# Performance work log

Hardware: AMD Instinct MI355X
Metric: run time of the kernel (lower is better)

## Reference

```python
import jax, jax.numpy as jnp
import numpy as np

N = 4096          # nodes (= Mamba sequence length)
E_EDGES = 65536   # edges
D = 512           # dim_h (= d_inner, expand=1)
NEXP = 4          # num_experts (cfg.model.num_experts)
DSTATE = 16
DCONV = 4
DTRANK = 32       # ceil(D/16)
EPS = 1e-5


def _silu(x):
    return x * jax.nn.sigmoid(x)


def _bn(h, g, b):
    # BatchNorm1d over node axis (batch statistics)
    mu = h.mean(0)
    var = h.var(0)
    return (h - mu) * jax.lax.rsqrt(var + EPS) * g + b


def _mamba(u, in_w, conv_w, conv_b, x_w, dt_w, dt_b, A_log, Dp, out_w):
    # u: [L, D] single-sequence Mamba(d_model=D, d_state=16, d_conv=4, expand=1)
    L = u.shape[0]
    xz = u @ in_w                      # [L, 2D]
    xc, z = xz[:, :D], xz[:, D:]
    xp = jnp.pad(xc, ((DCONV - 1, 0), (0, 0)))
    xconv = conv_b
    for k in range(DCONV):             # depthwise causal conv, tiny fixed loop
        xconv = xconv + conv_w[:, k] * xp[k:k + L]
    xs = _silu(xconv)                  # [L, D]
    dbc = xs @ x_w                     # [L, DTRANK + 2*DSTATE]
    dt = jax.nn.softplus(dbc[:, :DTRANK] @ dt_w + dt_b)          # [L, D]
    Bm = dbc[:, DTRANK:DTRANK + DSTATE]                          # [L, S]
    Cm = dbc[:, DTRANK + DSTATE:]                                # [L, S]
    A = -jnp.exp(A_log)                                          # [D, S]
    dA = jnp.exp(dt[:, :, None] * A[None])                       # [L, D, S]
    dBu = dt[:, :, None] * Bm[:, None, :] * xs[:, :, None]       # [L, D, S]

    def step(hprev, inp):
        dA_t, dBu_t, C_t = inp
        hn = dA_t * hprev + dBu_t
        return hn, (hn * C_t[None, :]).sum(-1)

    _, ys = jax.lax.scan(step, jnp.zeros((D, DSTATE), u.dtype), (dA, dBu, Cm))
    y = ys + Dp * xs
    return (y * _silu(z)) @ out_w      # [L, D]


def setup_inputs() -> dict:
    key = jax.random.key(0)
    ks = jax.random.split(key, 24)
    s = 1.0 / np.sqrt(D)
    inp = {}
    inp['x'] = jax.random.normal(ks[0], (N, D), jnp.float32)
    inp['edge_index'] = jax.random.randint(ks[1], (2, E_EDGES), 0, N)
    inp['edge_attr'] = jax.random.normal(ks[2], (E_EDGES, D), jnp.float32)
    # GINE nn: Linear(D,D) -> ReLU -> Linear(D,D)
    inp['gin_w1'] = jax.random.normal(ks[3], (D, D)) * s
    inp['gin_b1'] = jnp.zeros((D,))
    inp['gin_w2'] = jax.random.normal(ks[4], (D, D)) * s
    inp['gin_b2'] = jnp.zeros((D,))
    # BatchNorms
    inp['bn1l_g'] = jnp.ones((D,)); inp['bn1l_b'] = jnp.zeros((D,))
    inp['bn1a_g'] = jnp.ones((D,)); inp['bn1a_b'] = jnp.zeros((D,))
    inp['bn2_g'] = jnp.ones((D,)); inp['bn2_b'] = jnp.zeros((D,))
    # gating MLP [D, D//2, NEXP]
    inp['gate_w1'] = jax.random.normal(ks[5], (D, D // 2)) * s
    inp['gate_b1'] = jnp.zeros((D // 2,))
    inp['gate_w2'] = jax.random.normal(ks[6], (D // 2, NEXP)) * (1.0 / np.sqrt(D // 2))
    inp['gate_b2'] = jnp.zeros((NEXP,))
    # stacked per-expert Mamba params
    inp['in_w'] = jax.random.normal(ks[7], (NEXP, D, 2 * D)) * s
    inp['conv_w'] = jax.random.normal(ks[8], (NEXP, D, DCONV)) * 0.5
    inp['conv_b'] = jnp.zeros((NEXP, D))
    inp['x_w'] = jax.random.normal(ks[9], (NEXP, D, DTRANK + 2 * DSTATE)) * s
    inp['dt_w'] = jax.random.normal(ks[10], (NEXP, DTRANK, D)) * (1.0 / np.sqrt(DTRANK))
    inp['dt_b'] = jax.random.normal(ks[11], (NEXP, D)) * 0.1 - 4.0
    A0 = jnp.log(jnp.arange(1, DSTATE + 1, dtype=jnp.float32))
    inp['A_log'] = jnp.broadcast_to(A0, (NEXP, D, DSTATE)).copy()
    inp['Dp'] = jnp.ones((NEXP, D))
    inp['out_w'] = jax.random.normal(ks[12], (NEXP, D, D)) * s
    # FFN
    inp['ff_w1'] = jax.random.normal(ks[13], (D, 2 * D)) * s
    inp['ff_b1'] = jnp.zeros((2 * D,))
    inp['ff_w2'] = jax.random.normal(ks[14], (2 * D, D)) * (1.0 / np.sqrt(2 * D))
    inp['ff_b2'] = jnp.zeros((D,))
    return inp


def reference(x, edge_index, edge_attr,
              gin_w1, gin_b1, gin_w2, gin_b2,
              bn1l_g, bn1l_b, bn1a_g, bn1a_b, bn2_g, bn2_b,
              gate_w1, gate_b1, gate_w2, gate_b2,
              in_w, conv_w, conv_b, x_w, dt_w, dt_b, A_log, Dp, out_w,
              ff_w1, ff_b1, ff_w2, ff_b2):
    h_in = x
    src, dst = edge_index[0], edge_index[1]
    # local GINEConv: nn(x + sum_j relu(x_j + e_ji))
    msg = jax.nn.relu(x[src] + edge_attr)                      # [E, D]
    aggr = jax.ops.segment_sum(msg, dst, num_segments=N)       # [N, D]
    h_local = jax.nn.relu((x + aggr) @ gin_w1 + gin_b1) @ gin_w2 + gin_b2
    h_local = _bn(h_in + h_local, bn1l_g, bn1l_b)
    # gated mixture of Mamba experts
    gate = jax.nn.softmax(jax.nn.relu(x @ gate_w1 + gate_b1) @ gate_w2 + gate_b2, axis=-1)  # [N, NEXP]
    ys = jax.vmap(_mamba, in_axes=(None, 0, 0, 0, 0, 0, 0, 0, 0, 0))(
        x, in_w, conv_w, conv_b, x_w, dt_w, dt_b, A_log, Dp, out_w)  # [NEXP, N, D]
    h_attn = jnp.einsum('ne,end->nd', gate, ys)
    h_attn = _bn(h_in + h_attn, bn1a_g, bn1a_b)
    # fuse + FFN
    h = h_local + h_attn
    ff = jax.nn.relu(h @ ff_w1 + ff_b1) @ ff_w2 + ff_b2
    return _bn(h + ff, bn2_g, bn2_b)
```

## Files before the change

kernel.cpp:

```cpp
#include <hip/hip_runtime.h>
#include <hip/hip_bf16.h>
#include <math.h>

#define N_NODES 4096
#define E_EDGE 65536
#define D 512
#define NEXP 4
#define DSTATE 16
#define DCONV 4
#define DTRANK 32
#define EPS 1e-5f
#define LCHUNK 64
#define NCHUNK (N_NODES / LCHUNK)

typedef __hip_bfloat16 bf16;
typedef short bf16x8 __attribute__((ext_vector_type(8)));
typedef float f32x4 __attribute__((ext_vector_type(4)));
typedef unsigned short u16x4 __attribute__((ext_vector_type(4)));

__device__ __forceinline__ float siluf(float x) { return x / (1.f + __expf(-x)); }
__device__ __forceinline__ float softplusf(float x) {
  return (x > 20.f) ? x : log1pf(__expf(x));
}
__device__ __forceinline__ unsigned short f2bf(float v) {
  bf16 b = __float2bfloat16(v);
  return *reinterpret_cast<unsigned short*>(&b);
}
__device__ __forceinline__ float bfu2f(unsigned short u) {
  bf16 b;
  *reinterpret_cast<unsigned short*>(&b) = u;
  return __bfloat162float(b);
}

__device__ __forceinline__ void gload16(const void* g, void* l) {
  __builtin_amdgcn_global_load_lds(
      (const __attribute__((address_space(1))) void*)g,
      (__attribute__((address_space(3))) void*)l, 16, 0, 0);
}

template <int FN, int EPI, bool STATS>
__global__ __launch_bounds__(256, 2) void mm_k(
    const bf16* __restrict__ A, int lda, long sA,
    const bf16* __restrict__ Bt, int ldb, long sB,
    const float* __restrict__ bias,
    float* __restrict__ Cf, bf16* __restrict__ Cb, int ldc, long sC, int K,
    const float* __restrict__ part, float* __restrict__ sacc) {
  constexpr int BN = FN * 32;
  __shared__ __align__(16) bf16 As[2][128 * 32];
  __shared__ __align__(16) bf16 Bs[2][BN * 32];
  const int z = blockIdx.z;
  A += (size_t)z * sA;
  Bt += (size_t)z * sB;
  const int tid = threadIdx.x;
  const int w = tid >> 6, l = tid & 63;
  const int wr = w >> 1, wc = w & 1;
  const int bm = blockIdx.y * 128, bn = blockIdx.x * BN;

  f32x4 acc[4][FN];
#pragma unroll
  for (int i = 0; i < 4; ++i)
#pragma unroll
    for (int j = 0; j < FN; ++j) acc[i][j] = 0.f;

  const int srow = l >> 2, schunk = l & 3;
  const bf16* gA = A + (size_t)(bm + w * 16 + srow) * lda + schunk * 8;
  const bf16* gB = Bt + (size_t)(bn + w * 16 + srow) * ldb + schunk * 8;

  const int ar = wr * 64 + (l & 15);
  const int br = wc * FN * 16 + (l & 15);
  const int kb = l >> 4;

  auto stage = [&](int b, int k0) {
    gload16(gA + k0, As[b] + w * 512);
    gload16(gA + k0 + (size_t)64 * lda, As[b] + 64 * 32 + w * 512);
    gload16(gB + k0, Bs[b] + w * 512);
    if (FN == 4) gload16(gB + k0 + (size_t)64 * ldb, Bs[b] + 64 * 32 + w * 512);
  };

  stage(0, 0);
  __syncthreads();
  int cur = 0;
  for (int k0 = 0; k0 < K; k0 += 32) {
    if (k0 + 32 < K) stage(cur ^ 1, k0 + 32);
    const bf16x8* Ap = (const bf16x8*)As[cur];
    const bf16x8* Bp = (const bf16x8*)Bs[cur];
    bf16x8 af[4], bfr[FN];
#pragma unroll
    for (int i = 0; i < 4; ++i) af[i] = Ap[(ar + i * 16) * 4 + kb];
#pragma unroll
    for (int j = 0; j < FN; ++j) bfr[j] = Bp[(br + j * 16) * 4 + kb];
#pragma unroll
    for (int i = 0; i < 4; ++i)
#pragma unroll
      for (int j = 0; j < FN; ++j)
        acc[i][j] = __builtin_amdgcn_mfma_f32_16x16x32_bf16(bfr[j], af[i], acc[i][j], 0, 0, 0);
    __syncthreads();
    cur ^= 1;
  }

  if (Cf) Cf += (size_t)z * sC;
  if (Cb) Cb += (size_t)z * sC;
  const int r0 = bm + wr * 64 + (l & 15);
  const int cb0 = bn + wc * FN * 16 + ((l >> 4) << 2);
  f32x4 ssum[FN], ssq[FN];
  if (STATS) {
#pragma unroll
    for (int j = 0; j < FN; ++j) { ssum[j] = 0.f; ssq[j] = 0.f; }
  }
#pragma unroll
  for (int i = 0; i < 4; ++i) {
    const int row = r0 + i * 16;
#pragma unroll
    for (int j = 0; j < FN; ++j) {
      const int col = cb0 + j * 16;
      f32x4 v = acc[i][j];
      if (bias) v += *(const f32x4*)&bias[col];
      if (EPI == 1) {
#pragma unroll
        for (int r = 0; r < 4; ++r) v[r] = fmaxf(v[r], 0.f);
      }
      if (Cf) *(f32x4*)&Cf[(size_t)row * ldc + col] = v;
      if (Cb) {
        u16x4 u;
#pragma unroll
        for (int r = 0; r < 4; ++r) u[r] = f2bf(v[r]);
        *(u16x4*)&Cb[(size_t)row * ldc + col] = u;
      }
      if (STATS) {
        f32x4 p = *(const f32x4*)&part[(size_t)row * ldc + col];
        f32x4 t = v + p;
        ssum[j] += t;
        ssq[j] += t * t;
      }
    }
  }
  if (STATS) {
#pragma unroll
    for (int m = 1; m < 16; m <<= 1) {
#pragma unroll
      for (int j = 0; j < FN; ++j)
#pragma unroll
        for (int r = 0; r < 4; ++r) {
          ssum[j][r] += __shfl_xor(ssum[j][r], m);
          ssq[j][r] += __shfl_xor(ssq[j][r], m);
        }
    }
    if ((l & 15) == 0) {
#pragma unroll
      for (int j = 0; j < FN; ++j)
#pragma unroll
        for (int r = 0; r < 4; ++r) {
          atomicAdd(&sacc[cb0 + j * 16 + r], ssum[j][r]);
          atomicAdd(&sacc[512 + cb0 + j * 16 + r], ssq[j][r]);
        }
    }
  }
}

__global__ __launch_bounds__(256, 2) void g1pack_k(
    const bf16* __restrict__ hpre, const bf16* __restrict__ xbf,
    const bf16* __restrict__ gw1t, const bf16* __restrict__ catw,
    const float* __restrict__ gin_b1, const float* __restrict__ gate_b1,
    bf16* __restrict__ t1, float* __restrict__ g1, bf16* __restrict__ xz) {
  __shared__ __align__(16) bf16 As[2][128 * 32];
  __shared__ __align__(16) bf16 Bs[2][128 * 32];
  const int b = blockIdx.x;
  const bool isGin = b < 128;
  int bm, bnBase;
  const bf16 *A, *Bt;
  if (isGin) {
    bm = (b >> 2) * 128;
    bnBase = (b & 3) * 128;
    A = hpre;
    Bt = gw1t + (size_t)bnBase * 512;
  } else {
    const int local = b - 128;
    bm = (local / 34) * 128;
    bnBase = (local % 34) * 128;
    A = xbf;
    Bt = catw + (size_t)bnBase * 512;
  }
  const int tid = threadIdx.x;
  const int w = tid >> 6, l = tid & 63;
  const int wr = w >> 1, wc = w & 1;

  f32x4 acc[4][4];
#pragma unroll
  for (int i = 0; i < 4; ++i)
#pragma unroll
    for (int j = 0; j < 4; ++j) acc[i][j] = 0.f;

  const int srow = l >> 2, schunk = l & 3;
  const bf16* gA = A + (size_t)(bm + w * 16 + srow) * 512 + schunk * 8;
  const bf16* gB = Bt + (size_t)(w * 16 + srow) * 512 + schunk * 8;

  const int ar = wr * 64 + (l & 15);
  const int br = wc * 64 + (l & 15);
  const int kb = l >> 4;

  auto stage = [&](int bb, int k0) {
    gload16(gA + k0, As[bb] + w * 512);
    gload16(gA + k0 + (size_t)64 * 512, As[bb] + 64 * 32 + w * 512);
    gload16(gB + k0, Bs[bb] + w * 512);
    gload16(gB + k0 + (size_t)64 * 512, Bs[bb] + 64 * 32 + w * 512);
  };

  stage(0, 0);
  __syncthreads();
  int cur = 0;
  for (int k0 = 0; k0 < 512; k0 += 32) {
    if (k0 + 32 < 512) stage(cur ^ 1, k0 + 32);
    const bf16x8* Ap = (const bf16x8*)As[cur];
    const bf16x8* Bp = (const bf16x8*)Bs[cur];
    bf16x8 af[4], bfr[4];
#pragma unroll
    for (int i = 0; i < 4; ++i) af[i] = Ap[(ar + i * 16) * 4 + kb];
#pragma unroll
    for (int j = 0; j < 4; ++j) bfr[j] = Bp[(br + j * 16) * 4 + kb];
#pragma unroll
    for (int i = 0; i < 4; ++i)
#pragma unroll
      for (int j = 0; j < 4; ++j)
        acc[i][j] = __builtin_amdgcn_mfma_f32_16x16x32_bf16(bfr[j], af[i], acc[i][j], 0, 0, 0);
    __syncthreads();
    cur ^= 1;
  }

  const int r0 = bm + wr * 64 + (l & 15);
  const int c0 = wc * 64 + ((l >> 4) << 2);
  const bool isGate = (!isGin) && (bnBase < 256);
  bf16* xz_e = nullptr;
  int co_base = 0;
  if (!isGin && !isGate) {
    const int e = (bnBase - 256) >> 10;
    xz_e = xz + (size_t)e * N_NODES * 1024;
    co_base = (bnBase - 256) & 1023;
  }
#pragma unroll
  for (int i = 0; i < 4; ++i) {
    const int row = r0 + i * 16;
#pragma unroll
    for (int j = 0; j < 4; ++j) {
      const int ct = c0 + j * 16;
      f32x4 v = acc[i][j];
      if (isGin) {
        const int col = bnBase + ct;
        v += *(const f32x4*)&gin_b1[col];
        u16x4 u;
#pragma unroll
        for (int r = 0; r < 4; ++r) u[r] = f2bf(fmaxf(v[r], 0.f));
        *(u16x4*)&t1[(size_t)row * 512 + col] = u;
      } else if (isGate) {
        const int col = bnBase + ct;
        v += *(const f32x4*)&gate_b1[col];
#pragma unroll
        for (int r = 0; r < 4; ++r) v[r] = fmaxf(v[r], 0.f);
        *(f32x4*)&g1[(size_t)row * 256 + col] = v;
      } else {
        const int co = co_base + ct;
        u16x4 u;
#pragma unroll
        for (int r = 0; r < 4; ++r) u[r] = f2bf(v[r]);
        *(u16x4*)&xz_e[(size_t)row * 1024 + co] = u;
      }
    }
  }
}

struct MmArgs {
  const bf16* A[4];
  const bf16* Bt[4];
  const float* bias[4];
  float* Cf[4];
  bf16* Cb[4];
  const float* part[4];
  float* sacc[4];
  long sA[4], sB[4], sC[4];
  int lda[4], ldb[4], ldc[4], K[4], epi[4], stats[4], gx[4], cum[4];
};
__global__ __launch_bounds__(256, 2) void mgemm_k(MmArgs a) {
  __shared__ __align__(16) bf16 As[2][128 * 32];
  __shared__ __align__(16) bf16 Bs[2][64 * 32];
  int b = blockIdx.x;
  int i = 0;
  while (b >= a.cum[i]) ++i;
  int local = b - (i ? a.cum[i - 1] : 0);
  const int perz = a.gx[i] * 32;
  const int z = local / perz;
  const int rem = local - z * perz;
  const int by = rem / a.gx[i];
  const int bx = rem - by * a.gx[i];
  const int lda = a.lda[i], ldb = a.ldb[i], ldc = a.ldc[i], K = a.K[i];
  const bf16* A = a.A[i] + (size_t)z * a.sA[i];
  const bf16* Bt = a.Bt[i] + (size_t)z * a.sB[i];

  const int tid = threadIdx.x;
  const int w = tid >> 6, l = tid & 63;
  const int wr = w >> 1, wc = w & 1;
  const int bm = by * 128, bn = bx * 64;

  f32x4 acc[4][2];
#pragma unroll
  for (int p = 0; p < 4; ++p)
#pragma unroll
    for (int j = 0; j < 2; ++j) acc[p][j] = 0.f;

  const int srow = l >> 2, schunk = l & 3;
  const bf16* gA = A + (size_t)(bm + w * 16 + srow) * lda + schunk * 8;
  const bf16* gB = Bt + (size_t)(bn + w * 16 + srow) * ldb + schunk * 8;

  const int ar = wr * 64 + (l & 15);
  const int br = wc * 32 + (l & 15);
  const int kb = l >> 4;

  auto stage = [&](int bb, int k0) {
    gload16(gA + k0, As[bb] + w * 512);
    gload16(gA + k0 + (size_t)64 * lda, As[bb] + 64 * 32 + w * 512);
    gload16(gB + k0, Bs[bb] + w * 512);
  };

  stage(0, 0);
  __syncthreads();
  int cur = 0;
  for (int k0 = 0; k0 < K; k0 += 32) {
    if (k0 + 32 < K) stage(cur ^ 1, k0 + 32);
    const bf16x8* Ap = (const bf16x8*)As[cur];
    const bf16x8* Bp = (const bf16x8*)Bs[cur];
    bf16x8 af[4], bfr[2];
#pragma unroll
    for (int p = 0; p < 4; ++p) af[p] = Ap[(ar + p * 16) * 4 + kb];
#pragma unroll
    for (int j = 0; j < 2; ++j) bfr[j] = Bp[(br + j * 16) * 4 + kb];
#pragma unroll
    for (int p = 0; p < 4; ++p)
#pragma unroll
      for (int j = 0; j < 2; ++j)
        acc[p][j] = __builtin_amdgcn_mfma_f32_16x16x32_bf16(bfr[j], af[p], acc[p][j], 0, 0, 0);
    __syncthreads();
    cur ^= 1;
  }

  float* Cf = a.Cf[i] ? a.Cf[i] + (size_t)z * a.sC[i] : nullptr;
  bf16* Cb = a.Cb[i] ? a.Cb[i] + (size_t)z * a.sC[i] : nullptr;
  const float* bias = a.bias[i];
  const int epi = a.epi[i], stats = a.stats[i];
  const int r0 = bm + wr * 64 + (l & 15);
  const int cb0 = bn + wc * 32 + ((l >> 4) << 2);
  f32x4 ssum[2], ssq[2];
  ssum[0] = 0.f; ssum[1] = 0.f; ssq[0] = 0.f; ssq[1] = 0.f;
#pragma unroll
  for (int p = 0; p < 4; ++p) {
    const int row = r0 + p * 16;
#pragma unroll
    for (int j = 0; j < 2; ++j) {
      const int col = cb0 + j * 16;
      f32x4 v = acc[p][j];
      if (bias) v += *(const f32x4*)&bias[col];
      if (epi == 1) {
#pragma unroll
        for (int r = 0; r < 4; ++r) v[r] = fmaxf(v[r], 0.f);
      }
      if (Cf) *(f32x4*)&Cf[(size_t)row * ldc + col] = v;
      if (Cb) {
        u16x4 u;
#pragma unroll
        for (int r = 0; r < 4; ++r) u[r] = f2bf(v[r]);
        *(u16x4*)&Cb[(size_t)row * ldc + col] = u;
      }
      if (stats) {
        f32x4 pp = *(const f32x4*)&a.part[i][(size_t)row * ldc + col];
        f32x4 t = v + pp;
        ssum[j] += t;
        ssq[j] += t * t;
      }
    }
  }
  if (stats) {
#pragma unroll
    for (int m = 1; m < 16; m <<= 1) {
#pragma unroll
      for (int j = 0; j < 2; ++j)
#pragma unroll
        for (int r = 0; r < 4; ++r) {
          ssum[j][r] += __shfl_xor(ssum[j][r], m);
          ssq[j][r] += __shfl_xor(ssq[j][r], m);
        }
    }
    if ((l & 15) == 0) {
#pragma unroll
      for (int j = 0; j < 2; ++j)
#pragma unroll
        for (int r = 0; r < 4; ++r) {
          atomicAdd(&a.sacc[i][cb0 + j * 16 + r], ssum[j][r]);
          atomicAdd(&a.sacc[i][512 + cb0 + j * 16 + r], ssq[j][r]);
        }
    }
  }
}

struct WtArgs {
  const float* in[8];
  bf16* out[8];
  int K[8], N[8], ldo[8];
  long sin[8], sout[8];
  int cum[8];
};
__global__ __launch_bounds__(256) void wtrans_all_k(WtArgs a) {
  __shared__ float t[32][33];
  int b = blockIdx.x;
  int i = 0;
  while (b >= a.cum[i]) ++i;
  int local = b - (i ? a.cum[i - 1] : 0);
  const int ntx = a.N[i] / 32;
  const int nty = a.K[i] / 32;
  const int perz = ntx * nty;
  const int z = local / perz;
  const int rem = local - z * perz;
  const int bx = rem % ntx, by = rem / ntx;
  const float* in = a.in[i] + (size_t)z * a.sin[i];
  bf16* out = a.out[i] + (size_t)z * a.sout[i];
  const int N = a.N[i], ldo = a.ldo[i];
  const int n0 = bx * 32, k0 = by * 32;
  const int tx = threadIdx.x & 31, ty = threadIdx.x >> 5;
  for (int r = ty; r < 32; r += 8) t[r][tx] = in[(size_t)(k0 + r) * N + n0 + tx];
  __syncthreads();
  for (int r = ty; r < 32; r += 8)
    out[(size_t)(n0 + r) * ldo + k0 + tx] = __float2bfloat16(t[tx][r]);
}

__global__ void hist_k(const int* __restrict__ ei, int* __restrict__ deg) {
  int e = blockIdx.x * 256 + threadIdx.x;
  if (e < E_EDGE) atomicAdd(&deg[ei[E_EDGE + e]], 1);
}

__global__ __launch_bounds__(1024) void prefix_k(const int* __restrict__ deg,
                                                 int* __restrict__ rowstart) {
  __shared__ int s[1024];
  int t = threadIdx.x;
  int base = t * 4;
  int d0 = deg[base], d1 = deg[base + 1], d2 = deg[base + 2], d3 = deg[base + 3];
  int sum = d0 + d1 + d2 + d3;
  s[t] = sum;
  __syncthreads();
  for (int off = 1; off < 1024; off <<= 1) {
    int v = (t >= off) ? s[t - off] : 0;
    __syncthreads();
    s[t] += v;
    __syncthreads();
  }
  int excl = s[t] - sum;
  rowstart[base] = excl;
  rowstart[base + 1] = excl + d0;
  rowstart[base + 2] = excl + d0 + d1;
  rowstart[base + 3] = excl + d0 + d1 + d2;
}

__global__ void scatter_k(const int* __restrict__ ei, const int* __restrict__ rowstart,
                          int* __restrict__ cnt, int* __restrict__ eid) {
  int e = blockIdx.x * 256 + threadIdx.x;
  if (e < E_EDGE) {
    int dst = ei[E_EDGE + e];
    int slot = rowstart[dst] + atomicAdd(&cnt[dst], 1);
    eid[slot] = e;
  }
}

__global__ __launch_bounds__(256) void aggr_gather_k(
    const float* __restrict__ x, const int* __restrict__ ei, const float* __restrict__ ea,
    const int* __restrict__ rowstart, const int* __restrict__ deg,
    const int* __restrict__ eid, bf16* __restrict__ hpre, bf16* __restrict__ xbf) {
  __shared__ float comb[512];
  const int n = blockIdx.x;
  const int sub = threadIdx.x >> 7;
  const int lane = threadIdx.x & 127;
  const int d4 = lane << 2;
  const int beg = rowstart[n];
  const int end = beg + deg[n];
  f32x4 a = 0.f;
  for (int i = beg + sub; i < end; i += 2) {
    const int e = eid[i];
    const int s = ei[e];
    f32x4 xv = *(const f32x4*)&x[(size_t)s * D + d4];
    f32x4 ev = *(const f32x4*)&ea[(size_t)e * D + d4];
#pragma unroll
    for (int j = 0; j < 4; ++j) a[j] += fmaxf(xv[j] + ev[j], 0.f);
  }
  if (sub == 0) *(f32x4*)&comb[d4] = a;
  __syncthreads();
  if (sub == 1) {
    a += *(const f32x4*)&comb[d4];
    f32x4 xn = *(const f32x4*)&x[(size_t)n * D + d4];
    u16x4 h, xb;
#pragma unroll
    for (int j = 0; j < 4; ++j) {
      h[j] = f2bf(xn[j] + a[j]);
      xb[j] = f2bf(xn[j]);
    }
    *(u16x4*)&hpre[(size_t)n * D + d4] = h;
    *(u16x4*)&xbf[(size_t)n * D + d4] = xb;
  }
}

__device__ __forceinline__ void gate2_body(const float* __restrict__ g1,
                                           const float* __restrict__ w2,
                                           const float* __restrict__ b2,
                                           float* __restrict__ gate, int blk) {
  int row = blk * 4 + (threadIdx.x >> 6);
  int lane = threadIdx.x & 63;
  float a0 = 0.f, a1 = 0.f, a2 = 0.f, a3 = 0.f;
  for (int k = lane; k < 256; k += 64) {
    float v = g1[(size_t)row * 256 + k];
    a0 = fmaf(v, w2[k * 4 + 0], a0);
    a1 = fmaf(v, w2[k * 4 + 1], a1);
    a2 = fmaf(v, w2[k * 4 + 2], a2);
    a3 = fmaf(v, w2[k * 4 + 3], a3);
  }
#pragma unroll
  for (int off = 32; off; off >>= 1) {
    a0 += __shfl_down(a0, off);
    a1 += __shfl_down(a1, off);
    a2 += __shfl_down(a2, off);
    a3 += __shfl_down(a3, off);
  }
  if (lane == 0) {
    float l0 = a0 + b2[0], l1 = a1 + b2[1], l2 = a2 + b2[2], l3 = a3 + b2[3];
    float m = fmaxf(fmaxf(l0, l1), fmaxf(l2, l3));
    float e0 = __expf(l0 - m), e1 = __expf(l1 - m), e2 = __expf(l2 - m), e3 = __expf(l3 - m);
    float s = 1.f / (e0 + e1 + e2 + e3);
    gate[row * 4 + 0] = e0 * s;
    gate[row * 4 + 1] = e1 * s;
    gate[row * 4 + 2] = e2 * s;
    gate[row * 4 + 3] = e3 * s;
  }
}

__global__ __launch_bounds__(256) void gate2_k(const float* __restrict__ g1,
                                               const float* __restrict__ w2,
                                               const float* __restrict__ b2,
                                               float* __restrict__ gate) {
  gate2_body(g1, w2, b2, gate, blockIdx.x);
}

__device__ __forceinline__ void conv_body(const bf16* __restrict__ xz,
                                          const float* __restrict__ cw,
                                          const float* __restrict__ cb,
                                          bf16* __restrict__ xs, int z, int e0, int bx) {
  xz += (size_t)z * N_NODES * 2 * D;
  xs += (size_t)z * N_NODES * D;
  cw += (size_t)(e0 + z) * D * DCONV;
  cb += (size_t)(e0 + z) * D;
  int idx = bx * 256 + threadIdx.x;
  if (idx >= N_NODES * (D / 4)) return;
  int t = idx >> 7;
  int d4 = (idx & 127) << 2;
  float a[4];
#pragma unroll
  for (int j = 0; j < 4; ++j) a[j] = cb[d4 + j];
#pragma unroll
  for (int k = 0; k < DCONV; ++k) {
    int tt = t + k - (DCONV - 1);
    if (tt >= 0) {
      u16x4 v = *(const u16x4*)&xz[(size_t)tt * (2 * D) + d4];
#pragma unroll
      for (int j = 0; j < 4; ++j) a[j] = fmaf(cw[(d4 + j) * DCONV + k], bfu2f(v[j]), a[j]);
    }
  }
  u16x4 o;
#pragma unroll
  for (int j = 0; j < 4; ++j) o[j] = f2bf(siluf(a[j]));
  *(u16x4*)&xs[(size_t)t * D + d4] = o;
}

__global__ void conv_silu_k(const bf16* __restrict__ xz, const float* __restrict__ cw,
                            const float* __restrict__ cb, bf16* __restrict__ xs, int e0) {
  conv_body(xz, cw, cb, xs, blockIdx.y, e0, blockIdx.x);
}

__global__ __launch_bounds__(256) void convgate_k(
    const bf16* __restrict__ xz, const float* __restrict__ cw,
    const float* __restrict__ cb, bf16* __restrict__ xs,
    const float* __restrict__ g1, const float* __restrict__ w2,
    const float* __restrict__ b2, float* __restrict__ gate) {
  if (blockIdx.y == 4) {
    if (blockIdx.x < N_NODES / 4) gate2_body(g1, w2, b2, gate, blockIdx.x);
    return;
  }
  conv_body(xz, cw, cb, xs, blockIdx.y, 0, blockIdx.x);
}

__device__ __forceinline__ void bn_params(const float* acc, int d, float& mu, float& rsig) {
  mu = acc[d] * (1.f / N_NODES);
  float var = acc[512 + d] * (1.f / N_NODES) - mu * mu;
  rsig = rsqrtf(var + EPS);
}

__global__ void norm_k(const float* __restrict__ p, const bf16* __restrict__ q,
                       const float* __restrict__ acc, const float* __restrict__ g,
                       const float* __restrict__ b, float* __restrict__ o) {
  int idx = blockIdx.x * blockDim.x + threadIdx.x;
  if (idx >= N_NODES * (D / 4)) return;
  int d4 = (idx & 127) << 2;
  size_t base = (size_t)idx << 2;
  f32x4 pv = *(const f32x4*)&p[base];
  u16x4 qv = *(const u16x4*)&q[base];
  f32x4 gv = *(const f32x4*)&g[d4];
  f32x4 bv = *(const f32x4*)&b[d4];
  f32x4 ov;
#pragma unroll
  for (int j = 0; j < 4; ++j) {
    float mu, rs;
    bn_params(acc, d4 + j, mu, rs);
    ov[j] = (pv[j] + bfu2f(qv[j]) - mu) * rs * gv[j] + bv[j];
  }
  *(f32x4*)&o[base] = ov;
}

__global__ void bnadd2_k(const float* __restrict__ x, const bf16* __restrict__ hloc,
                         const bf16* __restrict__ hattn, const float* __restrict__ acc1,
                         const float* __restrict__ acc2, const float* __restrict__ g1,
                         const float* __restrict__ b1, const float* __restrict__ g2,
                         const float* __restrict__ b2, float* __restrict__ of,
                         bf16* __restrict__ ob) {
  int idx = blockIdx.x * blockDim.x + threadIdx.x;
  if (idx >= N_NODES * (D / 4)) return;
  int d4 = (idx & 127) << 2;
  size_t base = (size_t)idx << 2;
  f32x4 xv = *(const f32x4*)&x[base];
  u16x4 hl = *(const u16x4*)&hloc[base];
  u16x4 ha = *(const u16x4*)&hattn[base];
  f32x4 g1v = *(const f32x4*)&g1[d4];
  f32x4 b1v = *(const f32x4*)&b1[d4];
  f32x4 g2v = *(const f32x4*)&g2[d4];
  f32x4 b2v = *(const f32x4*)&b2[d4];
  f32x4 ov;
  u16x4 obv;
#pragma unroll
  for (int j = 0; j < 4; ++j) {
    float mu1, rs1, mu2, rs2;
    bn_params(acc1, d4 + j, mu1, rs1);
    bn_params(acc2, d4 + j, mu2, rs2);
    float v = (xv[j] + bfu2f(hl[j]) - mu1) * rs1 * g1v[j] + b1v[j] +
              (xv[j] + bfu2f(ha[j]) - mu2) * rs2 * g2v[j] + b2v[j];
    ov[j] = v;
    obv[j] = f2bf(v);
  }
  *(f32x4*)&of[base] = ov;
  *(u16x4*)&ob[base] = obv;
}

__global__ __launch_bounds__(512) void scanA_k(const bf16* __restrict__ xs,
                                               const float* __restrict__ dbc,
                                               const float* __restrict__ Alog,
                                               const float* __restrict__ dtw,
                                               const float* __restrict__ dtbias,
                                               bf16* __restrict__ dtout,
                                               bf16* __restrict__ Q,
                                               float* __restrict__ dtsum, int e0) {
  const int z = blockIdx.y;
  xs += (size_t)z * N_NODES * D;
  dbc += (size_t)z * N_NODES * 64;
  Alog += (size_t)(e0 + z) * D * DSTATE;
  dtw += (size_t)(e0 + z) * DTRANK * D;
  dtbias += (size_t)(e0 + z) * D;
  dtout += (size_t)z * N_NODES * D;
  Q += (size_t)z * NCHUNK * D * DSTATE;
  dtsum += (size_t)z * NCHUNK * D;
  int c = blockIdx.x;
  int d = threadIdx.x;
  float wv[DTRANK];
#pragma unroll
  for (int k = 0; k < DTRANK; ++k) wv[k] = dtw[k * D + d];
  const float dtb0 = dtbias[d];
  float As[DSTATE], h[DSTATE];
#pragma unroll
  for (int s = 0; s < DSTATE; ++s) {
    As[s] = -__expf(Alog[d * DSTATE + s]);
    h[s] = 0.f;
  }
  float dts = 0.f;
  int t0 = c * LCHUNK;
  for (int t = t0; t < t0 + LCHUNK; ++t) {
    float acc = dtb0;
#pragma unroll
    for (int k = 0; k < DTRANK; ++k) acc = fmaf(dbc[(size_t)t * 64 + k], wv[k], acc);
    bf16 dtb16 = __float2bfloat16(softplusf(acc));
    dtout[(size_t)t * D + d] = dtb16;
    float dtv = __bfloat162float(dtb16);
    float xv = __bfloat162float(xs[(size_t)t * D + d]);
    float bx = dtv * xv;
    dts += dtv;
#pragma unroll
    for (int s = 0; s < DSTATE; ++s) {
      float Bv = dbc[(size_t)t * 64 + DTRANK + s];
      h[s] = fmaf(__expf(dtv * As[s]), h[s], bx * Bv);
    }
  }
  size_t base = ((size_t)c * D + d) * DSTATE;
#pragma unroll
  for (int q4 = 0; q4 < 4; ++q4) {
    u16x4 u;
#pragma unroll
    for (int r = 0; r < 4; ++r) u[r] = f2bf(h[q4 * 4 + r]);
    *(u16x4*)&Q[base + q4 * 4] = u;
  }
  dtsum[c * D + d] = dts;
}

__global__ __launch_bounds__(256) void scanB_k(const bf16* __restrict__ Q,
                                               const float* __restrict__ dtsum,
                                               const float* __restrict__ Alog,
                                               bf16* __restrict__ Hin, int e0) {
  const int z = blockIdx.y;
  Q += (size_t)z * NCHUNK * D * DSTATE;
  dtsum += (size_t)z * NCHUNK * D;
  Alog += (size_t)(e0 + z) * D * DSTATE;
  Hin += (size_t)z * NCHUNK * D * DSTATE;
  int idx = blockIdx.x * blockDim.x + threadIdx.x;
  int d = idx >> 4;
  float As = -__expf(Alog[idx]);
  float h = 0.f;
  for (int c = 0; c < NCHUNK; ++c) {
    size_t base = (size_t)c * D * DSTATE + idx;
    Hin[base] = __float2bfloat16(h);
    h = fmaf(__expf(As * dtsum[c * D + d]), h, __bfloat162float(Q[base]));
  }
}

__global__ __launch_bounds__(512) void scanC_k(const bf16* __restrict__ dt,
                                               const bf16* __restrict__ xs,
                                               const float* __restrict__ dbc,
                                               const float* __restrict__ Alog,
                                               const bf16* __restrict__ Hin,
                                               const bf16* __restrict__ xz,
                                               const float* __restrict__ Dp,
                                               const float* __restrict__ gate,
                                               bf16* __restrict__ u, int e0) {
  const int z = blockIdx.y;
  dt += (size_t)z * N_NODES * D;
  xs += (size_t)z * N_NODES * D;
  dbc += (size_t)z * N_NODES * 64;
  Alog += (size_t)(e0 + z) * D * DSTATE;
  Hin += (size_t)z * NCHUNK * D * DSTATE;
  xz += (size_t)z * N_NODES * 2 * D;
  Dp += (size_t)(e0 + z) * D;
  u += (size_t)(e0 + z) * 512;
  const int ge = e0 + z;
  int c = blockIdx.x;
  int d = threadIdx.x;
  float As[DSTATE], h[DSTATE];
  size_t base = ((size_t)c * D + d) * DSTATE;
#pragma unroll
  for (int s = 0; s < DSTATE; ++s) {
    As[s] = -__expf(Alog[d * DSTATE + s]);
    h[s] = __bfloat162float(Hin[base + s]);
  }
  float Dv = Dp[d];
  int t0 = c * LCHUNK;
  for (int t = t0; t < t0 + LCHUNK; ++t) {
    float dtv = __bfloat162float(dt[(size_t)t * D + d]);
    float xv = __bfloat162float(xs[(size_t)t * D + d]);
    float bx = dtv * xv;
    float y = 0.f;
#pragma unroll
    for (int s = 0; s < DSTATE; ++s) {
      float Bv = dbc[(size_t)t * 64 + DTRANK + s];
      float Cv = dbc[(size_t)t * 64 + DTRANK + DSTATE + s];
      h[s] = fmaf(__expf(dtv * As[s]), h[s], bx * Bv);
      y = fmaf(h[s], Cv, y);
    }
    float zv = __bfloat162float(xz[(size_t)t * (2 * D) + D + d]);
    float gv = gate[t * NEXP + ge];
    u[(size_t)t * 2048 + d] = __float2bfloat16(gv * (y + Dv * xv) * siluf(zv));
  }
}

extern "C" void kernel_launch(void* const* d_in, const int* in_sizes, int n_in,
                              void* d_out, int out_size, void* d_ws, size_t ws_size,
                              hipStream_t stream) {
  const float* x = (const float*)d_in[0];
  const int* ei = (const int*)d_in[1];
  const float* ea = (const float*)d_in[2];
  const float* gin_w1 = (const float*)d_in[3];
  const float* gin_b1 = (const float*)d_in[4];
  const float* gin_w2 = (const float*)d_in[5];
  const float* gin_b2 = (const float*)d_in[6];
  const float* bn1l_g = (const float*)d_in[7];
  const float* bn1l_b = (const float*)d_in[8];
  const float* bn1a_g = (const float*)d_in[9];
  const float* bn1a_b = (const float*)d_in[10];
  const float* bn2_g = (const float*)d_in[11];
  const float* bn2_b = (const float*)d_in[12];
  const float* gate_w1 = (const float*)d_in[13];
  const float* gate_b1 = (const float*)d_in[14];
  const float* gate_w2 = (const float*)d_in[15];
  const float* gate_b2 = (const float*)d_in[16];
  const float* in_w = (const float*)d_in[17];
  const float* conv_w = (const float*)d_in[18];
  const float* conv_b = (const float*)d_in[19];
  const float* x_w = (const float*)d_in[20];
  const float* dt_w = (const float*)d_in[21];
  const float* dt_b = (const float*)d_in[22];
  const float* A_log = (const float*)d_in[23];
  const float* Dp = (const float*)d_in[24];
  const float* out_w = (const float*)d_in[25];
  const float* ff_w1 = (const float*)d_in[26];
  const float* ff_b1 = (const float*)d_in[27];
  const float* ff_w2 = (const float*)d_in[28];
  const float* ff_b2 = (const float*)d_in[29];
  float* out = (float*)d_out;

  const size_t ND = (size_t)N_NODES * D;
  const size_t NDb = ND / 2;
  const size_t QH = (size_t)NCHUNK * D * DSTATE / 2;

  const size_t fixed_f = 3 * ND + (size_t)N_NODES * 256 + 16384 + 2490624 + ND + 2048 +
                         81920 + 2 * ND + 4096;
  const size_t per_f = 2 * ND + NDb + (size_t)N_NODES * 64 + NDb + 2 * QH +
                       (size_t)NCHUNK * D;
  const int EB = (ws_size >= (fixed_f + 4 * per_f + 65536) * sizeof(float)) ? 4 : 1;

  float* ws = (float*)d_ws;
  size_t off = 0;
  auto alloc = [&](size_t n) {
    float* p = ws + off;
    off += (n + 63) & ~(size_t)63;
    return p;
  };
  float* ffo_f = alloc(ND);
  float* pbuf = alloc(ND);
  float* hlocal_f = alloc(ND);
  float* g1 = alloc((size_t)N_NODES * 256);
  float* gate = alloc((size_t)N_NODES * NEXP);
  bf16* gw1t = (bf16*)alloc(131072);
  bf16* gw2t = (bf16*)alloc(131072);
  bf16* catw = (bf16*)alloc(1114112);
  bf16* xwt = (bf16*)alloc(65536);
  bf16* outwt_cat = (bf16*)alloc(524288);
  bf16* ffw1t = (bf16*)alloc(262144);
  bf16* ffw2t = (bf16*)alloc(262144);
  int* deg = (int*)alloc(N_NODES);
  int* cnt = (int*)alloc(N_NODES);
  float* accs = alloc(3072);
  int* eid = (int*)alloc(E_EDGE);
  int* rowstart = (int*)alloc(N_NODES);
  float* xbf_f = alloc(NDb);
  float* xz_f = alloc((size_t)EB * ND);
  float* xs_f = alloc((size_t)EB * NDb);
  float* dbc = alloc((size_t)EB * N_NODES * 64);
  float* dtb_f = alloc((size_t)EB * NDb);
  float* Qb_f = alloc((size_t)EB * QH);
  float* Hin_f = alloc((size_t)EB * QH);
  float* dtsum = alloc((size_t)EB * NCHUNK * D);
  float* ucat_f = alloc(4 * NDb);
  float* hattn_f = alloc(ND);
  float* acc1 = accs, *acc2 = accs + 1024, *acc3 = accs + 2048;

  bf16* x_bf = (bf16*)xbf_f;
  bf16* hpre_bf = (bf16*)pbuf;
  bf16* t1_bf = (bf16*)(pbuf + NDb);
  bf16* xz_bf = (bf16*)xz_f;
  bf16* xs_bf = (bf16*)xs_f;
  bf16* dt_bf = (bf16*)dtb_f;
  bf16* Qb = (bf16*)Qb_f;
  bf16* Hin = (bf16*)Hin_f;
  bf16* ucat = (bf16*)ucat_f;
  bf16* hlocal_bf = (bf16*)hlocal_f;
  bf16* hattn_bf = (bf16*)hattn_f;
  bf16* ffo_bf = (bf16*)ffo_f;
  bf16* gatew1t = catw;
  bf16* inwt = catw + (size_t)256 * 512;
  float* hcomb = xz_f;
  bf16* hcomb_bf = (bf16*)(ucat_f);
  bf16* ffh_bf = (bf16*)pbuf;

  const int nelem = N_NODES * D;
  const int ew4 = (nelem / 4 + 255) / 256;

  hipMemsetAsync(deg, 0, (N_NODES + N_NODES + 3072) * sizeof(float), stream);

  WtArgs wa;
  const float* wsrc[8] = {gin_w1, gin_w2, gate_w1, in_w, x_w, out_w, ff_w1, ff_w2};
  bf16* wdst[8] = {gw1t, gw2t, catw, inwt, xwt, outwt_cat, ffw1t, ffw2t};
  int wK[8] = {512, 512, 512, 512, 512, 512, 512, 1024};
  int wN[8] = {512, 512, 256, 1024, 64, 512, 1024, 512};
  int wldo[8] = {512, 512, 512, 512, 512, 2048, 512, 1024};
  long wsin[8] = {0, 0, 0, (long)512 * 1024, (long)512 * 64, (long)512 * 512, 0, 0};
  long wsout[8] = {0, 0, 0, (long)1024 * 512, (long)64 * 512, 512, 0, 0};
  int wz[8] = {1, 1, 1, 4, 4, 4, 1, 1};
  int cum = 0;
  for (int i = 0; i < 8; ++i) {
    wa.in[i] = wsrc[i];
    wa.out[i] = wdst[i];
    wa.K[i] = wK[i];
    wa.N[i] = wN[i];
    wa.ldo[i] = wldo[i];
    wa.sin[i] = wsin[i];
    wa.sout[i] = wsout[i];
    cum += (wN[i] / 32) * (wK[i] / 32) * wz[i];
    wa.cum[i] = cum;
  }
  wtrans_all_k<<<cum, 256, 0, stream>>>(wa);

  hist_k<<<E_EDGE / 256, 256, 0, stream>>>(ei, deg);
  prefix_k<<<1, 1024, 0, stream>>>(deg, rowstart);
  scatter_k<<<E_EDGE / 256, 256, 0, stream>>>(ei, rowstart, cnt, eid);
  aggr_gather_k<<<N_NODES, 256, 0, stream>>>(x, ei, ea, rowstart, deg, eid, hpre_bf, x_bf);

  if (EB == 4) {
    g1pack_k<<<1216, 256, 0, stream>>>(hpre_bf, x_bf, gw1t, catw, gin_b1, gate_b1,
                                       t1_bf, g1, xz_bf);
    convgate_k<<<dim3(ew4, 5), 256, 0, stream>>>(xz_bf, conv_w, conv_b, xs_bf, g1,
                                                 gate_w2, gate_b2, gate);

    MmArgs m2 = {};
    m2.A[0] = t1_bf; m2.lda[0] = 512; m2.sA[0] = 0;
    m2.Bt[0] = gw2t; m2.ldb[0] = 512; m2.sB[0] = 0;
    m2.bias[0] = gin_b2; m2.Cb[0] = hlocal_bf; m2.ldc[0] = 512; m2.sC[0] = 0;
    m2.K[0] = 512; m2.epi[0] = 0; m2.stats[0] = 1; m2.part[0] = x; m2.sacc[0] = acc1;
    m2.gx[0] = 8;
    m2.A[1] = xs_bf; m2.lda[1] = 512; m2.sA[1] = (long)ND;
    m2.Bt[1] = xwt; m2.ldb[1] = 512; m2.sB[1] = (long)64 * 512;
    m2.Cf[1] = dbc; m2.ldc[1] = 64; m2.sC[1] = (long)N_NODES * 64;
    m2.K[1] = 512; m2.epi[1] = 0; m2.gx[1] = 1;
    int c2 = 8 * 32;
    m2.cum[0] = c2;
    c2 += 1 * 32 * 4;
    m2.cum[1] = c2;
    m2.cum[2] = c2;
    m2.cum[3] = c2;
    mgemm_k<<<c2, 256, 0, stream>>>(m2);

    scanA_k<<<dim3(NCHUNK, 4), 512, 0, stream>>>(xs_bf, dbc, A_log, dt_w, dt_b, dt_bf,
                                                 Qb, dtsum, 0);
    scanB_k<<<dim3((D * DSTATE) / 256, 4), 256, 0, stream>>>(Qb, dtsum, A_log, Hin, 0);
    scanC_k<<<dim3(NCHUNK, 4), 512, 0, stream>>>(dt_bf, xs_bf, dbc, A_log, Hin, xz_bf, Dp,
                                                 gate, ucat, 0);
  } else {
    mm_k<2, 1, false><<<dim3(8, 32, 1), 256, 0, stream>>>(
        hpre_bf, 512, 0, gw1t, 512, 0, gin_b1, nullptr, t1_bf, 512, 0, 512, nullptr,
        nullptr);
    mm_k<2, 0, true><<<dim3(8, 32, 1), 256, 0, stream>>>(
        t1_bf, 512, 0, gw2t, 512, 0, gin_b2, nullptr, hlocal_bf, 512, 0, 512, x, acc1);
    mm_k<2, 1, false><<<dim3(4, 32, 1), 256, 0, stream>>>(
        x_bf, 512, 0, gatew1t, 512, 0, gate_b1, g1, nullptr, 256, 0, 512, nullptr,
        nullptr);
    gate2_k<<<N_NODES / 4, 256, 0, stream>>>(g1, gate_w2, gate_b2, gate);
    for (int e0 = 0; e0 < NEXP; ++e0) {
      mm_k<4, 0, false><<<dim3(8, 32, 1), 256, 0, stream>>>(
          x_bf, 512, 0, inwt + (size_t)e0 * 1024 * 512, 512, 0, nullptr, nullptr, xz_bf,
          1024, 0, 512, nullptr, nullptr);
      conv_silu_k<<<dim3(ew4, 1), 256, 0, stream>>>(xz_bf, conv_w, conv_b, xs_bf, e0);
      mm_k<2, 0, false><<<dim3(1, 32, 1), 256, 0, stream>>>(
          xs_bf, 512, 0, xwt + (size_t)e0 * 64 * 512, 512, 0, nullptr, dbc, nullptr, 64,
          0, 512, nullptr, nullptr);
      scanA_k<<<dim3(NCHUNK, 1), 512, 0, stream>>>(xs_bf, dbc, A_log, dt_w, dt_b, dt_bf,
                                                   Qb, dtsum, e0);
      scanB_k<<<dim3((D * DSTATE) / 256, 1), 256, 0, stream>>>(Qb, dtsum, A_log, Hin, e0);
      scanC_k<<<dim3(NCHUNK, 1), 512, 0, stream>>>(dt_bf, xs_bf, dbc, A_log, Hin, xz_bf,
                                                   Dp, gate, ucat, e0);
    }
  }

  mm_k<2, 0, true><<<dim3(8, 32, 1), 256, 0, stream>>>(
      ucat, 2048, 0, outwt_cat, 2048, 0, nullptr, nullptr, hattn_bf, 512, 0, 2048, x,
      acc2);

  bnadd2_k<<<ew4, 256, 0, stream>>>(x, hlocal_bf, hattn_bf, acc1, acc2, bn1l_g, bn1l_b,
                                    bn1a_g, bn1a_b, hcomb, hcomb_bf);
  mm_k<4, 1, false><<<dim3(8, 32, 1), 256, 0, stream>>>(
      hcomb_bf, 512, 0, ffw1t, 512, 0, ff_b1, nullptr, ffh_bf, 1024, 0, 512, nullptr,
      nullptr);
  mm_k<2, 0, true><<<dim3(8, 32, 1), 256, 0, stream>>>(
      ffh_bf, 1024, 0, ffw2t, 1024, 0, ff_b2, nullptr, ffo_bf, 512, 0, 1024, hcomb, acc3);
  norm_k<<<ew4, 256, 0, stream>>>(hcomb, ffo_bf, acc3, bn2_g, bn2_b, out);
}
```

Before: 424.1 us.

## Recompute dt in scanC and store dbc in bf16 instead of materializing dt

scanA no longer writes the [N, D] bf16 dt tensor per expert. scanC recomputes dt from the low-rank dbc projection with per-thread dt_w weights. The x_proj GEMM output dbc is now stored as bf16 rather than fp32, halving its footprint and read traffic in both scan kernels. This removes an N×D write and read per expert at the cost of a 32-FMA dot product plus softplus per element in scanC, and adds bf16 rounding on the B/C/dt-rank inputs.

```diff
diff --git a/kernel.cpp b/kernel.cpp
--- a/kernel.cpp
+++ b/kernel.cpp
@@ -649,11 +649,10 @@
 }
 
 __global__ __launch_bounds__(512) void scanA_k(const bf16* __restrict__ xs,
-                                               const float* __restrict__ dbc,
+                                               const bf16* __restrict__ dbc,
                                                const float* __restrict__ Alog,
                                                const float* __restrict__ dtw,
                                                const float* __restrict__ dtbias,
-                                               bf16* __restrict__ dtout,
                                                bf16* __restrict__ Q,
                                                float* __restrict__ dtsum, int e0) {
   const int z = blockIdx.y;
@@ -662,7 +661,6 @@
   Alog += (size_t)(e0 + z) * D * DSTATE;
   dtw += (size_t)(e0 + z) * DTRANK * D;
   dtbias += (size_t)(e0 + z) * D;
-  dtout += (size_t)z * N_NODES * D;
   Q += (size_t)z * NCHUNK * D * DSTATE;
   dtsum += (size_t)z * NCHUNK * D;
   int c = blockIdx.x;
@@ -682,16 +680,15 @@
   for (int t = t0; t < t0 + LCHUNK; ++t) {
     float acc = dtb0;
 #pragma unroll
-    for (int k = 0; k < DTRANK; ++k) acc = fmaf(dbc[(size_t)t * 64 + k], wv[k], acc);
-    bf16 dtb16 = __float2bfloat16(softplusf(acc));
-    dtout[(size_t)t * D + d] = dtb16;
-    float dtv = __bfloat162float(dtb16);
+    for (int k = 0; k < DTRANK; ++k)
+      acc = fmaf(__bfloat162float(dbc[(size_t)t * 64 + k]), wv[k], acc);
+    float dtv = __bfloat162float(__float2bfloat16(softplusf(acc)));
     float xv = __bfloat162float(xs[(size_t)t * D + d]);
     float bx = dtv * xv;
     dts += dtv;
 #pragma unroll
     for (int s = 0; s < DSTATE; ++s) {
-      float Bv = dbc[(size_t)t * 64 + DTRANK + s];
+      float Bv = __bfloat162float(dbc[(size_t)t * 64 + DTRANK + s]);
       h[s] = fmaf(__expf(dtv * As[s]), h[s], bx * Bv);
     }
   }
@@ -726,20 +723,22 @@
   }
 }
 
-__global__ __launch_bounds__(512) void scanC_k(const bf16* __restrict__ dt,
-                                               const bf16* __restrict__ xs,
-                                               const float* __restrict__ dbc,
+__global__ __launch_bounds__(512) void scanC_k(const bf16* __restrict__ xs,
+                                               const bf16* __restrict__ dbc,
                                                const float* __restrict__ Alog,
+                                               const float* __restrict__ dtw,
+                                               const float* __restrict__ dtbias,
                                                const bf16* __restrict__ Hin,
                                                const bf16* __restrict__ xz,
                                                const float* __restrict__ Dp,
                                                const float* __restrict__ gate,
                                                bf16* __restrict__ u, int e0) {
   const int z = blockIdx.y;
-  dt += (size_t)z * N_NODES * D;
   xs += (size_t)z * N_NODES * D;
   dbc += (size_t)z * N_NODES * 64;
   Alog += (size_t)(e0 + z) * D * DSTATE;
+  dtw += (size_t)(e0 + z) * DTRANK * D;
+  dtbias += (size_t)(e0 + z) * D;
   Hin += (size_t)z * NCHUNK * D * DSTATE;
   xz += (size_t)z * N_NODES * 2 * D;
   Dp += (size_t)(e0 + z) * D;
@@ -747,6 +746,10 @@
   const int ge = e0 + z;
   int c = blockIdx.x;
   int d = threadIdx.x;
+  float wv[DTRANK];
+#pragma unroll
+  for (int k = 0; k < DTRANK; ++k) wv[k] = dtw[k * D + d];
+  const float dtb0 = dtbias[d];
   float As[DSTATE], h[DSTATE];
   size_t base = ((size_t)c * D + d) * DSTATE;
 #pragma unroll
@@ -757,14 +760,18 @@
   float Dv = Dp[d];
   int t0 = c * LCHUNK;
   for (int t = t0; t < t0 + LCHUNK; ++t) {
-    float dtv = __bfloat162float(dt[(size_t)t * D + d]);
+    float acc = dtb0;
+#pragma unroll
+    for (int k = 0; k < DTRANK; ++k)
+      acc = fmaf(__bfloat162float(dbc[(size_t)t * 64 + k]), wv[k], acc);
+    float dtv = __bfloat162float(__float2bfloat16(softplusf(acc)));
     float xv = __bfloat162float(xs[(size_t)t * D + d]);
     float bx = dtv * xv;
     float y = 0.f;
 #pragma unroll
     for (int s = 0; s < DSTATE; ++s) {
-      float Bv = dbc[(size_t)t * 64 + DTRANK + s];
-      float Cv = dbc[(size_t)t * 64 + DTRANK + DSTATE + s];
+      float Bv = __bfloat162float(dbc[(size_t)t * 64 + DTRANK + s]);
+      float Cv = __bfloat162float(dbc[(size_t)t * 64 + DTRANK + DSTATE + s]);
       h[s] = fmaf(__expf(dtv * As[s]), h[s], bx * Bv);
       y = fmaf(h[s], Cv, y);
     }
@@ -815,7 +822,7 @@
 
   const size_t fixed_f = 3 * ND + (size_t)N_NODES * 256 + 16384 + 2490624 + ND + 2048 +
                          81920 + 2 * ND + 4096;
-  const size_t per_f = 2 * ND + NDb + (size_t)N_NODES * 64 + NDb + 2 * QH +
+  const size_t per_f = 2 * ND + NDb + (size_t)N_NODES * 32 + 2 * QH +
                        (size_t)NCHUNK * D;
   const int EB = (ws_size >= (fixed_f + 4 * per_f + 65536) * sizeof(float)) ? 4 : 1;
 
@@ -846,8 +853,7 @@
   float* xbf_f = alloc(NDb);
   float* xz_f = alloc((size_t)EB * ND);
   float* xs_f = alloc((size_t)EB * NDb);
-  float* dbc = alloc((size_t)EB * N_NODES * 64);
-  float* dtb_f = alloc((size_t)EB * NDb);
+  float* dbc_f = alloc((size_t)EB * N_NODES * 32);
   float* Qb_f = alloc((size_t)EB * QH);
   float* Hin_f = alloc((size_t)EB * QH);
   float* dtsum = alloc((size_t)EB * NCHUNK * D);
@@ -860,7 +866,7 @@
   bf16* t1_bf = (bf16*)(pbuf + NDb);
   bf16* xz_bf = (bf16*)xz_f;
   bf16* xs_bf = (bf16*)xs_f;
-  bf16* dt_bf = (bf16*)dtb_f;
+  bf16* dbc_bf = (bf16*)dbc_f;
   bf16* Qb = (bf16*)Qb_f;
   bf16* Hin = (bf16*)Hin_f;
   bf16* ucat = (bf16*)ucat_f;
@@ -920,7 +926,7 @@
     m2.gx[0] = 8;
     m2.A[1] = xs_bf; m2.lda[1] = 512; m2.sA[1] = (long)ND;
     m2.Bt[1] = xwt; m2.ldb[1] = 512; m2.sB[1] = (long)64 * 512;
-    m2.Cf[1] = dbc; m2.ldc[1] = 64; m2.sC[1] = (long)N_NODES * 64;
+    m2.Cb[1] = dbc_bf; m2.ldc[1] = 64; m2.sC[1] = (long)N_NODES * 64;
     m2.K[1] = 512; m2.epi[1] = 0; m2.gx[1] = 1;
     int c2 = 8 * 32;
     m2.cum[0] = c2;
@@ -930,11 +936,11 @@
     m2.cum[3] = c2;
     mgemm_k<<<c2, 256, 0, stream>>>(m2);
 
-    scanA_k<<<dim3(NCHUNK, 4), 512, 0, stream>>>(xs_bf, dbc, A_log, dt_w, dt_b, dt_bf,
+    scanA_k<<<dim3(NCHUNK, 4), 512, 0, stream>>>(xs_bf, dbc_bf, A_log, dt_w, dt_b,
                                                  Qb, dtsum, 0);
     scanB_k<<<dim3((D * DSTATE) / 256, 4), 256, 0, stream>>>(Qb, dtsum, A_log, Hin, 0);
-    scanC_k<<<dim3(NCHUNK, 4), 512, 0, stream>>>(dt_bf, xs_bf, dbc, A_log, Hin, xz_bf, Dp,
-                                                 gate, ucat, 0);
+    scanC_k<<<dim3(NCHUNK, 4), 512, 0, stream>>>(xs_bf, dbc_bf, A_log, dt_w, dt_b, Hin,
+                                                 xz_bf, Dp, gate, ucat, 0);
   } else {
     mm_k<2, 1, false><<<dim3(8, 32, 1), 256, 0, stream>>>(
         hpre_bf, 512, 0, gw1t, 512, 0, gin_b1, nullptr, t1_bf, 512, 0, 512, nullptr,
@@ -951,13 +957,13 @@
           1024, 0, 512, nullptr, nullptr);
       conv_silu_k<<<dim3(ew4, 1), 256, 0, stream>>>(xz_bf, conv_w, conv_b, xs_bf, e0);
       mm_k<2, 0, false><<<dim3(1, 32, 1), 256, 0, stream>>>(
-          xs_bf, 512, 0, xwt + (size_t)e0 * 64 * 512, 512, 0, nullptr, dbc, nullptr, 64,
-          0, 512, nullptr, nullptr);
-      scanA_k<<<dim3(NCHUNK, 1), 512, 0, stream>>>(xs_bf, dbc, A_log, dt_w, dt_b, dt_bf,
+          xs_bf, 512, 0, xwt + (size_t)e0 * 64 * 512, 512, 0, nullptr, nullptr, dbc_bf,
+          64, 0, 512, nullptr, nullptr);
+      scanA_k<<<dim3(NCHUNK, 1), 512, 0, stream>>>(xs_bf, dbc_bf, A_log, dt_w, dt_b,
                                                    Qb, dtsum, e0);
       scanB_k<<<dim3((D * DSTATE) / 256, 1), 256, 0, stream>>>(Qb, dtsum, A_log, Hin, e0);
-      scanC_k<<<dim3(NCHUNK, 1), 512, 0, stream>>>(dt_bf, xs_bf, dbc, A_log, Hin, xz_bf,
-                                                   Dp, gate, ucat, e0);
+      scanC_k<<<dim3(NCHUNK, 1), 512, 0, stream>>>(xs_bf, dbc_bf, A_log, dt_w, dt_b, Hin,
+                                                   xz_bf, Dp, gate, ucat, e0);
     }
   }
 
```

After: 478.4 us. 12.8% more time.
